# Performance work log

Measured on AMD Instinct MI355X. Metric: run time of the kernel, lower is better.

## Reference

```python
import jax, jax.numpy as jnp
import numpy as np

EPS = 1e-5  # BatchNorm3d default eps


def setup_inputs() -> dict:
    key = jax.random.key(0)
    ks = jax.random.split(key, 8)
    B, C, T, H, W = 2, 256, 8, 28, 28
    P, NS = 128, 5
    sc = 0.02  # keep activations stable through 5 residual stages
    return {
        "x": jax.random.normal(ks[0], (B, C, T, H, W), jnp.float32),
        "Wt": jax.random.normal(ks[1], (P, C), jnp.float32) * sc,
        "Wp": jax.random.normal(ks[2], (P, C), jnp.float32) * sc,
        "Wg": jax.random.normal(ks[3], (NS, P, C), jnp.float32) * sc,
        "W1": jax.random.normal(ks[4], (NS, C, P), jnp.float32) * sc,
        "W2": jax.random.normal(ks[5], (NS, C, P), jnp.float32) * sc,
        "gamma": jnp.ones((NS, C), jnp.float32),
        "beta": jnp.zeros((NS, C), jnp.float32),
    }


def _batchnorm(x, g, b):
    # x: [B, C, S]; training-mode BN over (batch, spatial) per channel
    mu = jnp.mean(x, axis=(0, 2), keepdims=True)
    var = jnp.var(x, axis=(0, 2), keepdims=True)
    xn = (x - mu) * jax.lax.rsqrt(var + EPS)
    return xn * g[None, :, None] + b[None, :, None]


def reference(x, Wt, Wp, Wg, W1, W2, gamma, beta):
    B, C, T, H, W = x.shape
    S = T * H * W
    xf = x.reshape(B, C, S)                      # [B,C,S]
    # DotKernel: att[b,i,j] = softmax_j( t[b,i,:] . p[b,:,j] )
    t = jnp.einsum("bcs,pc->bsp", xf, Wt)        # [B,S,P]
    p = jnp.einsum("bcs,pc->bps", xf, Wp)        # [B,P,S]
    att = jax.nn.softmax(jnp.einsum("bsp,bpq->bsq", t, p), axis=-1)  # [B,S,S]

    out = xf
    n_stages = Wg.shape[0]
    for i in range(n_stages):  # small fixed stage count
        g = jnp.einsum("bcs,pc->bsp", out, Wg[i])          # [B,S,P]
        x1 = jnp.einsum("bsp,cp->bcs", g, W1[i])           # w_1(g)
        x2 = jnp.einsum("bsq,bqp->bsp", att, g)            # att @ g
        x2 = jnp.einsum("bsp,cp->bcs", x2, W2[i])          # w_2(...)
        out = _batchnorm(x1 + x2, gamma[i], beta[i]) + out  # BN + residual
    return out.reshape(B, C, T, H, W)
```

## Files before the change

### kernel.cpp

```cpp
#include <hip/hip_runtime.h>

#define B_  2
#define C_  256
#define S_  6272
#define P_  128
#define NS_ 5
#define KS_ 7
#define KCH_ 896
#define EPS_ 1e-5f

typedef __attribute__((ext_vector_type(8))) short short8;
typedef __attribute__((ext_vector_type(4))) float f32x4;

__device__ __forceinline__ ushort f2bf(float f) {
    union { float f; unsigned u; } v; v.f = f;
    unsigned r = v.u + 0x7fffu + ((v.u >> 16) & 1u);
    return (ushort)(r >> 16);
}
__device__ __forceinline__ float bf2f(ushort h) {
    union { unsigned u; float f; } v; v.u = ((unsigned)h) << 16;
    return v.f;
}

__device__ __forceinline__ void gload16(const ushort* g, ushort* lds) {
    __builtin_amdgcn_global_load_lds(
        (const __attribute__((address_space(1))) void*)g,
        (__attribute__((address_space(3))) void*)lds, 16, 0, 0);
}

__global__ void k_convert_weights(const float* __restrict__ Wt, const float* __restrict__ Wp,
                                  const float* __restrict__ Wg, const float* __restrict__ W1,
                                  const float* __restrict__ W2,
                                  ushort* __restrict__ Wtpb,
                                  ushort* __restrict__ Wgb, ushort* __restrict__ catb) {
    int i = blockIdx.x * 256 + threadIdx.x;
    const int nWtp = 2 * P_ * C_;
    const int nWg  = NS_ * P_ * C_;
    const int nCat = NS_ * C_ * 2 * P_;
    if (i < nWtp) {
        int c = i & (C_ - 1), row = i >> 8;
        float v = (row < P_) ? Wt[row * C_ + c] : Wp[(row - P_) * C_ + c];
        Wtpb[i] = f2bf(v);
    }
    if (i < nWg) { Wgb[i] = f2bf(Wg[i]); }
    if (i < nCat) {
        int k  = i & 255;
        int c  = (i >> 8) & (C_ - 1);
        int st = i >> 16;
        float v = (k < P_) ? W1[((size_t)st * C_ + c) * P_ + k]
                           : W2[((size_t)st * C_ + c) * P_ + (k - P_)];
        catb[i] = f2bf(v);
    }
}

__global__ void k_init_x(const float* __restrict__ x, float* __restrict__ out,
                         ushort* __restrict__ xb_sc) {
    int bc = blockIdx.x;
    int b = bc / C_, c = bc - b * C_;
    const float* xr = x + (long)bc * S_;
    float* orow = out + (long)bc * S_;
    ushort* xs = xb_sc + (long)b * S_ * C_;
    for (int s = threadIdx.x; s < S_; s += 256) {
        float v = xr[s];
        orow[s] = v;
        xs[(long)s * C_ + c] = f2bf(v);
    }
}

template <int MODE>
__global__ __launch_bounds__(256, 2)
void k_gemm(const ushort* __restrict__ A, const ushort* __restrict__ Bm,
            void* __restrict__ Out, ushort* __restrict__ OutT,
            int M, int N, int K, int lda, int ldb, int ldo, int ldot,
            long sA, long sB, long sO, long sOT, int nks, int kch) {
    const int z = blockIdx.z;
    const int b = z / nks, ch = z - b * nks;
    A  += (long)b * sA;
    Bm += (long)b * sB;
    const int k0 = ch * kch, k1 = k0 + kch;

    const int bm = blockIdx.x * 128, bn = blockIdx.y * 128;

    __shared__ ushort Al[128][32];
    __shared__ ushort Bl[128][32];

    const int tid = threadIdx.x, lane = tid & 63, wid = tid >> 6;
    const int wr = (wid >> 1) * 64, wc = (wid & 1) * 64;
    const int r16 = lane & 15, kg = lane >> 4;

    const int st_row = lane >> 2;
    const int st_slot = lane & 3;
    const int st_gk8 = ((st_slot ^ ((st_row >> 1) & 3)) << 3);
    const int sw8 = ((kg ^ ((r16 >> 1) & 3)) << 3);

    const ushort* Arow0 = A + (long)(bm + wid * 32 + st_row) * lda + st_gk8;
    const ushort* Arow1 = A + (long)(bm + wid * 32 + 16 + st_row) * lda + st_gk8;
    const ushort* Brow0 = Bm + (long)(bn + wid * 32 + st_row) * ldb + st_gk8;
    const ushort* Brow1 = Bm + (long)(bn + wid * 32 + 16 + st_row) * ldb + st_gk8;

    f32x4 acc[4][4];
    #pragma unroll
    for (int i = 0; i < 4; ++i)
        #pragma unroll
        for (int j = 0; j < 4; ++j)
            acc[i][j] = (f32x4){0.f, 0.f, 0.f, 0.f};

    for (int kk = k0; kk < k1; kk += 32) {
        gload16(Arow0 + kk, &Al[wid * 32][0]);
        gload16(Arow1 + kk, &Al[wid * 32 + 16][0]);
        gload16(Brow0 + kk, &Bl[wid * 32][0]);
        gload16(Brow1 + kk, &Bl[wid * 32 + 16][0]);
        __syncthreads();

        short8 af[4], bfv[4];
        #pragma unroll
        for (int i = 0; i < 4; ++i)
            af[i] = *(const short8*)&Al[wr + i * 16 + r16][sw8];
        #pragma unroll
        for (int j = 0; j < 4; ++j)
            bfv[j] = *(const short8*)&Bl[wc + j * 16 + r16][sw8];

        #pragma unroll
        for (int i = 0; i < 4; ++i)
            #pragma unroll
            for (int j = 0; j < 4; ++j)
                acc[i][j] = __builtin_amdgcn_mfma_f32_16x16x32_bf16(af[i], bfv[j], acc[i][j], 0, 0, 0);
        __syncthreads();
    }

    const int orow0 = bm + wr + kg * 4;
    const int ocol0 = bn + wc + r16;
    if (MODE == 2) {
        float* O = (float*)Out + (long)z * sO;
        #pragma unroll
        for (int i = 0; i < 4; ++i)
            #pragma unroll
            for (int j = 0; j < 4; ++j)
                #pragma unroll
                for (int q = 0; q < 4; ++q)
                    O[(long)(orow0 + i * 16 + q) * ldo + (ocol0 + j * 16)] = acc[i][j][q];
    } else {
        ushort* O = (ushort*)Out + (long)z * sO;
        ushort* OT = (MODE == 1) ? (OutT + (long)z * sOT) : nullptr;
        #pragma unroll
        for (int i = 0; i < 4; ++i)
            #pragma unroll
            for (int j = 0; j < 4; ++j)
                #pragma unroll
                for (int q = 0; q < 4; ++q) {
                    ushort h = f2bf(acc[i][j][q]);
                    O[(long)(orow0 + i * 16 + q) * ldo + (ocol0 + j * 16)] = h;
                    if (MODE == 1)
                        OT[(long)(ocol0 + j * 16) * ldot + (orow0 + i * 16 + q)] = h;
                }
    }
}

__global__ __launch_bounds__(256)
void k_softmax(ushort* __restrict__ att) {
    long row = blockIdx.x;
    ushort* r = att + row * (long)S_;
    const int tid = threadIdx.x;
    __shared__ float red1[4];
    __shared__ float red2[4];
    const bool tail = tid < 16;

    short8 u0 = *(const short8*)&r[(0 * 256 + tid) * 8];
    short8 u1 = *(const short8*)&r[(1 * 256 + tid) * 8];
    short8 u2 = *(const short8*)&r[(2 * 256 + tid) * 8];
    short8 u3 = tail ? *(const short8*)&r[(768 + tid) * 8] : short8{0,0,0,0,0,0,0,0};

    float v[32];
    #pragma unroll
    for (int j = 0; j < 8; ++j) {
        v[j]      = bf2f((ushort)u0[j]);
        v[8 + j]  = bf2f((ushort)u1[j]);
        v[16 + j] = bf2f((ushort)u2[j]);
        v[24 + j] = tail ? bf2f((ushort)u3[j]) : -1e30f;
    }
    float mx = -1e30f;
    #pragma unroll
    for (int j = 0; j < 32; ++j) mx = fmaxf(mx, v[j]);
    #pragma unroll
    for (int off = 32; off; off >>= 1) mx = fmaxf(mx, __shfl_xor(mx, off));
    if ((tid & 63) == 0) red1[tid >> 6] = mx;
    __syncthreads();
    mx = fmaxf(fmaxf(red1[0], red1[1]), fmaxf(red1[2], red1[3]));

    float sum = 0.f;
    #pragma unroll
    for (int j = 0; j < 32; ++j) {
        float e = __expf(v[j] - mx);
        v[j] = e;
        sum += e;
    }
    #pragma unroll
    for (int off = 32; off; off >>= 1) sum += __shfl_xor(sum, off);
    if ((tid & 63) == 0) red2[tid >> 6] = sum;
    __syncthreads();
    sum = red2[0] + red2[1] + red2[2] + red2[3];
    float inv = 1.f / sum;

    short8 w0, w1, w2, w3;
    #pragma unroll
    for (int j = 0; j < 8; ++j) {
        w0[j] = (short)f2bf(v[j] * inv);
        w1[j] = (short)f2bf(v[8 + j] * inv);
        w2[j] = (short)f2bf(v[16 + j] * inv);
        w3[j] = (short)f2bf(v[24 + j] * inv);
    }
    *(short8*)&r[(0 * 256 + tid) * 8] = w0;
    *(short8*)&r[(1 * 256 + tid) * 8] = w1;
    *(short8*)&r[(2 * 256 + tid) * 8] = w2;
    if (tail) *(short8*)&r[(768 + tid) * 8] = w3;
}

__global__ void k_reduce_split(const float* __restrict__ split, ushort* __restrict__ BcatT) {
    long i = (long)blockIdx.x * 256 + threadIdx.x;
    if (i >= (long)B_ * S_ * P_) return;
    int p = (int)(i & (P_ - 1));
    long sp = i >> 7;
    int b = (int)(sp / S_);
    long s = sp - (long)b * S_;
    const float* base = split + (long)b * KS_ * S_ * P_ + s * P_ + p;
    float acc = 0.f;
    #pragma unroll
    for (int ch = 0; ch < KS_; ++ch) acc += base[(long)ch * S_ * P_];
    BcatT[((long)b * S_ + s) * 256 + 128 + p] = f2bf(acc);
}

__global__ __launch_bounds__(256)
void k_bn_stats(const float* __restrict__ y, float* __restrict__ mu, float* __restrict__ rs) {
    int c = blockIdx.x;
    const int tid = threadIdx.x;
    float s1 = 0.f, s2 = 0.f;
    for (int b = 0; b < B_; ++b) {
        const float* r = y + ((long)b * C_ + c) * S_;
        for (int s = tid; s < S_; s += 256) {
            float v = r[s];
            s1 += v;
            s2 += v * v;
        }
    }
    #pragma unroll
    for (int off = 32; off; off >>= 1) {
        s1 += __shfl_xor(s1, off);
        s2 += __shfl_xor(s2, off);
    }
    __shared__ float a1[4], a2[4];
    if ((tid & 63) == 0) { a1[tid >> 6] = s1; a2[tid >> 6] = s2; }
    __syncthreads();
    if (tid == 0) {
        s1 = a1[0] + a1[1] + a1[2] + a1[3];
        s2 = a2[0] + a2[1] + a2[2] + a2[3];
        const float invn = 1.f / (float)(B_ * S_);
        float m = s1 * invn;
        float var = s2 * invn - m * m;
        mu[c] = m;
        rs[c] = rsqrtf(var + EPS_);
    }
}

__global__ __launch_bounds__(256)
void k_bn_apply(const float* __restrict__ y, const float* __restrict__ mu,
                const float* __restrict__ rs, const float* __restrict__ gamma,
                const float* __restrict__ beta, float* __restrict__ out,
                ushort* __restrict__ xb_sc) {
    int bc = blockIdx.x;
    int b = bc / C_, c = bc - b * C_;
    float m = mu[c], r = rs[c], g = gamma[c], be = beta[c];
    const float* yr = y + (long)bc * S_;
    float* orow = out + (long)bc * S_;
    ushort* xs = xb_sc + (long)b * S_ * C_;
    for (int s = threadIdx.x; s < S_; s += 256) {
        float v = orow[s] + (yr[s] - m) * r * g + be;
        orow[s] = v;
        xs[(long)s * C_ + c] = f2bf(v);
    }
}

extern "C" void kernel_launch(void* const* d_in, const int* in_sizes, int n_in,
                              void* d_out, int out_size, void* d_ws, size_t ws_size,
                              hipStream_t stream) {
    const float* x     = (const float*)d_in[0];
    const float* Wt    = (const float*)d_in[1];
    const float* Wp    = (const float*)d_in[2];
    const float* Wg    = (const float*)d_in[3];
    const float* W1    = (const float*)d_in[4];
    const float* W2    = (const float*)d_in[5];
    const float* gamma = (const float*)d_in[6];
    const float* beta  = (const float*)d_in[7];
    float* out = (float*)d_out;

    char* ws = (char*)d_ws;
    size_t off = 0;
    auto alloc = [&](size_t bytes) -> void* {
        void* p = ws + off;
        off = (off + bytes + 255) & ~(size_t)255;
        return p;
    };
    ushort* att   = (ushort*)alloc((size_t)B_ * S_ * S_ * 2);
    ushort* tpb   = (ushort*)alloc((size_t)B_ * S_ * 256 * 2);
    ushort* gTb   = (ushort*)alloc((size_t)B_ * P_ * S_ * 2);
    ushort* BcatT = (ushort*)alloc((size_t)B_ * S_ * 256 * 2);
    ushort* xbsc  = (ushort*)alloc((size_t)B_ * S_ * C_ * 2);
    float*  y     = (float*)alloc((size_t)B_ * C_ * S_ * 4);
    float*  split = (float*)alloc((size_t)B_ * KS_ * S_ * P_ * 4);
    ushort* Wtpb  = (ushort*)alloc((size_t)2 * P_ * C_ * 2);
    ushort* Wgb   = (ushort*)alloc((size_t)NS_ * P_ * C_ * 2);
    ushort* catb  = (ushort*)alloc((size_t)NS_ * C_ * 256 * 2);
    float*  mu    = (float*)alloc(C_ * 4);
    float*  rs    = (float*)alloc(C_ * 4);
    if (off > ws_size) return;

    dim3 blk(256);

    k_convert_weights<<<1280, 256, 0, stream>>>(Wt, Wp, Wg, W1, W2, Wtpb, Wgb, catb);
    k_init_x<<<B_ * C_, 256, 0, stream>>>(x, out, xbsc);

    k_gemm<0><<<dim3(S_ / 128, 2, B_), blk, 0, stream>>>(
        xbsc, Wtpb, tpb, nullptr, S_, 256, C_, C_, C_, 256, 0,
        (long)S_ * C_, 0, (long)S_ * 256, 0, 1, C_);
    k_gemm<0><<<dim3(S_ / 128, S_ / 128, B_), blk, 0, stream>>>(
        tpb, tpb + 128, att, nullptr, S_, S_, P_, 256, 256, S_, 0,
        (long)S_ * 256, (long)S_ * 256, (long)S_ * S_, 0, 1, P_);
    k_softmax<<<B_ * S_, 256, 0, stream>>>(att);

    for (int i = 0; i < NS_; ++i) {
        k_gemm<1><<<dim3(S_ / 128, 1, B_), blk, 0, stream>>>(
            xbsc, Wgb + (size_t)i * P_ * C_, BcatT, gTb,
            S_, P_, C_, C_, C_, 256, S_,
            (long)S_ * C_, 0, (long)S_ * 256, (long)P_ * S_, 1, C_);
        k_gemm<2><<<dim3(S_ / 128, 1, B_ * KS_), blk, 0, stream>>>(
            att, gTb, split, nullptr, S_, P_, S_, S_, S_, P_, 0,
            (long)S_ * S_, (long)P_ * S_, (long)S_ * P_, 0, KS_, KCH_);
        k_reduce_split<<<(int)(((long)B_ * S_ * P_ + 255) / 256), 256, 0, stream>>>(split, BcatT);
        k_gemm<2><<<dim3(C_ / 128, S_ / 128, B_), blk, 0, stream>>>(
            catb + (size_t)i * C_ * 256, BcatT, y, nullptr,
            C_, S_, 256, 256, 256, S_, 0,
            0, (long)S_ * 256, (long)C_ * S_, 0, 1, 256);
        k_bn_stats<<<C_, 256, 0, stream>>>(y, mu, rs);
        k_bn_apply<<<B_ * C_, 256, 0, stream>>>(y, mu, rs, gamma + i * C_, beta + i * C_, out, xbsc);
    }
}
```

Before: 729.4 us.

## Fold split-K reduction into output GEMM and fuse BN statistics via atomics

The split-K partial products of att@g are now written as bf16 chunks side by side in a widened concatenated operand (K=640). The W2 weights are replicated across those chunks, so the final W1/W2 GEMM performs the split-K reduction itself and the separate reduce kernel and fp32 split buffer go away. The split count drops from 7 to 4. BN sum and sum-of-squares are accumulated in the final GEMM epilogue with shuffles and atomicAdd, which removes the separate stats kernel. The trade-offs are extra bf16 rounding of the partial sums, a larger K for the final GEMM, less parallelism in the att GEMM, and atomic contention.

```diff
diff --git a/kernel.cpp b/kernel.cpp
--- a/kernel.cpp
+++ b/kernel.cpp
@@ -5,8 +5,9 @@
 #define S_  6272
 #define P_  128
 #define NS_ 5
-#define KS_ 7
-#define KCH_ 896
+#define KS_ 4
+#define KCH_ 1568
+#define KY_ 640
 #define EPS_ 1e-5f
 
 typedef __attribute__((ext_vector_type(8))) short short8;
@@ -32,25 +33,27 @@
                                   const float* __restrict__ Wg, const float* __restrict__ W1,
                                   const float* __restrict__ W2,
                                   ushort* __restrict__ Wtpb,
-                                  ushort* __restrict__ Wgb, ushort* __restrict__ catb) {
+                                  ushort* __restrict__ Wgb, ushort* __restrict__ cat2b,
+                                  float* __restrict__ statb) {
     int i = blockIdx.x * 256 + threadIdx.x;
-    const int nWtp = 2 * P_ * C_;
-    const int nWg  = NS_ * P_ * C_;
-    const int nCat = NS_ * C_ * 2 * P_;
+    const int nWtp  = 2 * P_ * C_;
+    const int nWg   = NS_ * P_ * C_;
+    const int nCat2 = NS_ * C_ * KY_;
     if (i < nWtp) {
         int c = i & (C_ - 1), row = i >> 8;
         float v = (row < P_) ? Wt[row * C_ + c] : Wp[(row - P_) * C_ + c];
         Wtpb[i] = f2bf(v);
     }
     if (i < nWg) { Wgb[i] = f2bf(Wg[i]); }
-    if (i < nCat) {
-        int k  = i & 255;
-        int c  = (i >> 8) & (C_ - 1);
-        int st = i >> 16;
+    if (i < nCat2) {
+        int k  = i % KY_;
+        int c  = (i / KY_) & (C_ - 1);
+        int st = i / (KY_ * C_);
         float v = (k < P_) ? W1[((size_t)st * C_ + c) * P_ + k]
-                           : W2[((size_t)st * C_ + c) * P_ + (k - P_)];
-        catb[i] = f2bf(v);
-    }
+                           : W2[((size_t)st * C_ + c) * P_ + ((k - P_) & (P_ - 1))];
+        cat2b[i] = f2bf(v);
+    }
+    if (i < NS_ * 2 * C_) statb[i] = 0.f;
 }
 
 __global__ void k_init_x(const float* __restrict__ x, float* __restrict__ out,
@@ -70,9 +73,9 @@
 template <int MODE>
 __global__ __launch_bounds__(256, 2)
 void k_gemm(const ushort* __restrict__ A, const ushort* __restrict__ Bm,
-            void* __restrict__ Out, ushort* __restrict__ OutT,
+            void* __restrict__ Out, ushort* __restrict__ OutT, float* __restrict__ Stat,
             int M, int N, int K, int lda, int ldb, int ldo, int ldot,
-            long sA, long sB, long sO, long sOT, int nks, int kch) {
+            long sA, long sB, long sOb, long sOch, long sOT, int nks, int kch) {
     const int z = blockIdx.z;
     const int b = z / nks, ch = z - b * nks;
     A  += (long)b * sA;
@@ -130,8 +133,8 @@
 
     const int orow0 = bm + wr + kg * 4;
     const int ocol0 = bn + wc + r16;
-    if (MODE == 2) {
-        float* O = (float*)Out + (long)z * sO;
+    if (MODE == 3) {
+        float* O = (float*)Out + (long)b * sOb;
         #pragma unroll
         for (int i = 0; i < 4; ++i)
             #pragma unroll
@@ -139,9 +142,26 @@
                 #pragma unroll
                 for (int q = 0; q < 4; ++q)
                     O[(long)(orow0 + i * 16 + q) * ldo + (ocol0 + j * 16)] = acc[i][j][q];
+        #pragma unroll
+        for (int i = 0; i < 4; ++i)
+            #pragma unroll
+            for (int q = 0; q < 4; ++q) {
+                float s1 = acc[i][0][q] + acc[i][1][q] + acc[i][2][q] + acc[i][3][q];
+                float s2 = acc[i][0][q] * acc[i][0][q] + acc[i][1][q] * acc[i][1][q]
+                         + acc[i][2][q] * acc[i][2][q] + acc[i][3][q] * acc[i][3][q];
+                #pragma unroll
+                for (int off = 1; off < 16; off <<= 1) {
+                    s1 += __shfl_xor(s1, off);
+                    s2 += __shfl_xor(s2, off);
+                }
+                if (r16 == 0) {
+                    atomicAdd(&Stat[orow0 + i * 16 + q], s1);
+                    atomicAdd(&Stat[M + orow0 + i * 16 + q], s2);
+                }
+            }
     } else {
-        ushort* O = (ushort*)Out + (long)z * sO;
-        ushort* OT = (MODE == 1) ? (OutT + (long)z * sOT) : nullptr;
+        ushort* O = (ushort*)Out + (long)b * sOb + (long)ch * sOch;
+        ushort* OT = (MODE == 1) ? (OutT + (long)b * sOT) : nullptr;
         #pragma unroll
         for (int i = 0; i < 4; ++i)
             #pragma unroll
@@ -215,60 +235,18 @@
     if (tail) *(short8*)&r[(768 + tid) * 8] = w3;
 }
 
-__global__ void k_reduce_split(const float* __restrict__ split, ushort* __restrict__ BcatT) {
-    long i = (long)blockIdx.x * 256 + threadIdx.x;
-    if (i >= (long)B_ * S_ * P_) return;
-    int p = (int)(i & (P_ - 1));
-    long sp = i >> 7;
-    int b = (int)(sp / S_);
-    long s = sp - (long)b * S_;
-    const float* base = split + (long)b * KS_ * S_ * P_ + s * P_ + p;
-    float acc = 0.f;
-    #pragma unroll
-    for (int ch = 0; ch < KS_; ++ch) acc += base[(long)ch * S_ * P_];
-    BcatT[((long)b * S_ + s) * 256 + 128 + p] = f2bf(acc);
-}
-
 __global__ __launch_bounds__(256)
-void k_bn_stats(const float* __restrict__ y, float* __restrict__ mu, float* __restrict__ rs) {
-    int c = blockIdx.x;
-    const int tid = threadIdx.x;
-    float s1 = 0.f, s2 = 0.f;
-    for (int b = 0; b < B_; ++b) {
-        const float* r = y + ((long)b * C_ + c) * S_;
-        for (int s = tid; s < S_; s += 256) {
-            float v = r[s];
-            s1 += v;
-            s2 += v * v;
-        }
-    }
-    #pragma unroll
-    for (int off = 32; off; off >>= 1) {
-        s1 += __shfl_xor(s1, off);
-        s2 += __shfl_xor(s2, off);
-    }
-    __shared__ float a1[4], a2[4];
-    if ((tid & 63) == 0) { a1[tid >> 6] = s1; a2[tid >> 6] = s2; }
-    __syncthreads();
-    if (tid == 0) {
-        s1 = a1[0] + a1[1] + a1[2] + a1[3];
-        s2 = a2[0] + a2[1] + a2[2] + a2[3];
-        const float invn = 1.f / (float)(B_ * S_);
-        float m = s1 * invn;
-        float var = s2 * invn - m * m;
-        mu[c] = m;
-        rs[c] = rsqrtf(var + EPS_);
-    }
-}
-
-__global__ __launch_bounds__(256)
-void k_bn_apply(const float* __restrict__ y, const float* __restrict__ mu,
-                const float* __restrict__ rs, const float* __restrict__ gamma,
+void k_bn_apply(const float* __restrict__ y, const float* __restrict__ Stat,
+                const float* __restrict__ gamma,
                 const float* __restrict__ beta, float* __restrict__ out,
                 ushort* __restrict__ xb_sc) {
     int bc = blockIdx.x;
     int b = bc / C_, c = bc - b * C_;
-    float m = mu[c], r = rs[c], g = gamma[c], be = beta[c];
+    const float invn = 1.f / (float)(B_ * S_);
+    float m = Stat[c] * invn;
+    float var = Stat[C_ + c] * invn - m * m;
+    float r = rsqrtf(var + EPS_);
+    float g = gamma[c], be = beta[c];
     const float* yr = y + (long)bc * S_;
     float* orow = out + (long)bc * S_;
     ushort* xs = xb_sc + (long)b * S_ * C_;
@@ -302,44 +280,41 @@
     ushort* att   = (ushort*)alloc((size_t)B_ * S_ * S_ * 2);
     ushort* tpb   = (ushort*)alloc((size_t)B_ * S_ * 256 * 2);
     ushort* gTb   = (ushort*)alloc((size_t)B_ * P_ * S_ * 2);
-    ushort* BcatT = (ushort*)alloc((size_t)B_ * S_ * 256 * 2);
+    ushort* Bcat2 = (ushort*)alloc((size_t)B_ * S_ * KY_ * 2);
     ushort* xbsc  = (ushort*)alloc((size_t)B_ * S_ * C_ * 2);
     float*  y     = (float*)alloc((size_t)B_ * C_ * S_ * 4);
-    float*  split = (float*)alloc((size_t)B_ * KS_ * S_ * P_ * 4);
     ushort* Wtpb  = (ushort*)alloc((size_t)2 * P_ * C_ * 2);
     ushort* Wgb   = (ushort*)alloc((size_t)NS_ * P_ * C_ * 2);
-    ushort* catb  = (ushort*)alloc((size_t)NS_ * C_ * 256 * 2);
-    float*  mu    = (float*)alloc(C_ * 4);
-    float*  rs    = (float*)alloc(C_ * 4);
+    ushort* cat2b = (ushort*)alloc((size_t)NS_ * C_ * KY_ * 2);
+    float*  statb = (float*)alloc((size_t)NS_ * 2 * C_ * 4);
     if (off > ws_size) return;
 
     dim3 blk(256);
 
-    k_convert_weights<<<1280, 256, 0, stream>>>(Wt, Wp, Wg, W1, W2, Wtpb, Wgb, catb);
+    k_convert_weights<<<3200, 256, 0, stream>>>(Wt, Wp, Wg, W1, W2, Wtpb, Wgb, cat2b, statb);
     k_init_x<<<B_ * C_, 256, 0, stream>>>(x, out, xbsc);
 
     k_gemm<0><<<dim3(S_ / 128, 2, B_), blk, 0, stream>>>(
-        xbsc, Wtpb, tpb, nullptr, S_, 256, C_, C_, C_, 256, 0,
-        (long)S_ * C_, 0, (long)S_ * 256, 0, 1, C_);
+        xbsc, Wtpb, tpb, nullptr, nullptr, S_, 256, C_, C_, C_, 256, 0,
+        (long)S_ * C_, 0, (long)S_ * 256, 0, 0, 1, C_);
     k_gemm<0><<<dim3(S_ / 128, S_ / 128, B_), blk, 0, stream>>>(
-        tpb, tpb + 128, att, nullptr, S_, S_, P_, 256, 256, S_, 0,
-        (long)S_ * 256, (long)S_ * 256, (long)S_ * S_, 0, 1, P_);
+        tpb, tpb + 128, att, nullptr, nullptr, S_, S_, P_, 256, 256, S_, 0,
+        (long)S_ * 256, (long)S_ * 256, (long)S_ * S_, 0, 0, 1, P_);
     k_softmax<<<B_ * S_, 256, 0, stream>>>(att);
 
     for (int i = 0; i < NS_; ++i) {
         k_gemm<1><<<dim3(S_ / 128, 1, B_), blk, 0, stream>>>(
-            xbsc, Wgb + (size_t)i * P_ * C_, BcatT, gTb,
-            S_, P_, C_, C_, C_, 256, S_,
-            (long)S_ * C_, 0, (long)S_ * 256, (long)P_ * S_, 1, C_);
-        k_gemm<2><<<dim3(S_ / 128, 1, B_ * KS_), blk, 0, stream>>>(
-            att, gTb, split, nullptr, S_, P_, S_, S_, S_, P_, 0,
-            (long)S_ * S_, (long)P_ * S_, (long)S_ * P_, 0, KS_, KCH_);
-        k_reduce_split<<<(int)(((long)B_ * S_ * P_ + 255) / 256), 256, 0, stream>>>(split, BcatT);
-        k_gemm<2><<<dim3(C_ / 128, S_ / 128, B_), blk, 0, stream>>>(
-            catb + (size_t)i * C_ * 256, BcatT, y, nullptr,
-            C_, S_, 256, 256, 256, S_, 0,
-            0, (long)S_ * 256, (long)C_ * S_, 0, 1, 256);
-        k_bn_stats<<<C_, 256, 0, stream>>>(y, mu, rs);
-        k_bn_apply<<<B_ * C_, 256, 0, stream>>>(y, mu, rs, gamma + i * C_, beta + i * C_, out, xbsc);
-    }
-}
+            xbsc, Wgb + (size_t)i * P_ * C_, Bcat2, gTb, nullptr,
+            S_, P_, C_, C_, C_, KY_, S_,
+            (long)S_ * C_, 0, (long)S_ * KY_, 0, (long)P_ * S_, 1, C_);
+        k_gemm<0><<<dim3(S_ / 128, 1, B_ * KS_), blk, 0, stream>>>(
+            att, gTb, Bcat2 + 128, nullptr, nullptr, S_, P_, S_, S_, S_, KY_, 0,
+            (long)S_ * S_, (long)P_ * S_, (long)S_ * KY_, 128, 0, KS_, KCH_);
+        k_gemm<3><<<dim3(C_ / 128, S_ / 128, B_), blk, 0, stream>>>(
+            cat2b + (size_t)i * C_ * KY_, Bcat2, y, nullptr, statb + (size_t)i * 2 * C_,
+            C_, S_, KY_, KY_, KY_, S_, 0,
+            0, (long)S_ * KY_, (long)C_ * S_, 0, 0, 1, KY_);
+        k_bn_apply<<<B_ * C_, 256, 0, stream>>>(y, statb + (size_t)i * 2 * C_,
+                                                gamma + i * C_, beta + i * C_, out, xbsc);
+    }
+}
```

Result: slower. 779.2 us (+6.8%).
